# Kernel optimization log

Hardware: AMD Instinct MI355X
Metric: run time of the kernel (lower is better)

The kernel has to match this reference:

```python
import jax, jax.numpy as jnp
import numpy as np

B, N, FEAT = 64, 1024, 3
HID, STATE, LAYERS, NTYPES = 64, 32, 2, 10


def setup_inputs() -> dict:
    key = jax.random.key(0)
    ks = jax.random.split(key, 16)
    s = 0.1
    return {
        "task_features": jax.random.normal(ks[0], (B, N, FEAT), jnp.float32),
        "task_types": jax.random.randint(ks[1], (B, N), 0, NTYPES, jnp.int32),
        "prev_state": jnp.zeros((B, STATE), jnp.float32),
        "enc_w1": jax.random.normal(ks[2], (HID, FEAT), jnp.float32) * s,
        "enc_b1": jnp.zeros((HID,), jnp.float32),
        "enc_w2": jax.random.normal(ks[3], (HID, HID), jnp.float32) * s,
        "enc_b2": jnp.zeros((HID,), jnp.float32),
        "contention": jax.random.normal(ks[4], (NTYPES, NTYPES), jnp.float32) * 0.1,
        "gnn_w": jax.random.normal(ks[5], (LAYERS, HID, HID), jnp.float32) * s,
        "gnn_b": jnp.zeros((LAYERS, HID), jnp.float32),
        "gru_w_ih": jax.random.normal(ks[6], (3 * STATE, HID), jnp.float32) * s,
        "gru_w_hh": jax.random.normal(ks[7], (3 * STATE, STATE), jnp.float32) * s,
        "gru_b_ih": jnp.zeros((3 * STATE,), jnp.float32),
        "gru_b_hh": jnp.zeros((3 * STATE,), jnp.float32),
        "head_w1": jax.random.normal(ks[8], (HID, HID + STATE), jnp.float32) * s,
        "head_b1": jnp.zeros((HID,), jnp.float32),
        "head_w2": jax.random.normal(ks[9], (1, HID), jnp.float32) * s,
        "head_b2": jnp.zeros((1,), jnp.float32),
    }


def _forward(task_features, task_types, prev_state, enc_w1, enc_b1, enc_w2, enc_b2,
             contention, gnn_w, gnn_b, gru_w_ih, gru_w_hh, gru_b_ih, gru_b_hh,
             head_w1, head_b1, head_w2, head_b2):
    # task encoder: Linear -> ReLU -> Linear
    emb = jax.nn.relu(task_features @ enc_w1.T + enc_b1) @ enc_w2.T + enc_b2  # (B,N,H)
    # interaction graph: type-pair gather + cosine similarity
    base = contention[task_types[:, :, None], task_types[:, None, :]]  # (B,N,N)
    nrm = emb / jnp.maximum(jnp.linalg.norm(emb, axis=-1, keepdims=True), 1e-12)
    sim = jnp.einsum("bnd,bmd->bnm", nrm, nrm)
    adjacency = jax.nn.sigmoid(base) * sim  # (B,N,N)
    # GNN layers: aggregate + linear + relu
    h = emb
    for l in range(LAYERS):
        agg = jnp.einsum("bnm,bmd->bnd", adjacency, h)
        h = jax.nn.relu((h + agg) @ gnn_w[l].T + gnn_b[l])
    ctx = h.mean(axis=1)  # (B,H)
    # GRUCell (torch semantics)
    gi = ctx @ gru_w_ih.T + gru_b_ih
    gh = prev_state @ gru_w_hh.T + gru_b_hh
    i_r, i_z, i_n = jnp.split(gi, 3, axis=-1)
    h_r, h_z, h_n = jnp.split(gh, 3, axis=-1)
    r = jax.nn.sigmoid(i_r + h_r)
    z = jax.nn.sigmoid(i_z + h_z)
    n = jnp.tanh(i_n + r * h_n)
    new_state = (1.0 - z) * n + z * prev_state  # (B,S)
    # latency head on [h, state]
    st = jnp.broadcast_to(new_state[:, None, :], (h.shape[0], h.shape[1], new_state.shape[-1]))
    combined = jnp.concatenate([h, st], axis=-1)
    lat = jax.nn.relu(combined @ head_w1.T + head_b1) @ head_w2.T + head_b2
    return lat[..., 0], new_state


def reference(task_features, task_types, prev_state, enc_w1, enc_b1, enc_w2, enc_b2,
              contention, gnn_w, gnn_b, gru_w_ih, gru_w_hh, gru_b_ih, gru_b_hh,
              head_w1, head_b1, head_w2, head_b2):
    return _forward(task_features, task_types, prev_state, enc_w1, enc_b1, enc_w2, enc_b2,
                    contention, gnn_w, gnn_b, gru_w_ih, gru_w_hh, gru_b_ih, gru_b_hh,
                    head_w1, head_b1, head_w2, head_b2)
```

## Files before the change

kernel.cpp:

```cpp
#include <hip/hip_runtime.h>
#include <math.h>

#define BB 64
#define NN 1024
#define HID 64
#define STATE 32
#define NTYPES 10
#define CAP 256
#define CAPE (CAP * 64)

typedef _Float16 f16;
typedef f16 f16x8 __attribute__((ext_vector_type(8)));
typedef f16 f16x4 __attribute__((ext_vector_type(4)));
typedef float f32x4 __attribute__((ext_vector_type(4)));

#define MFMA16(a, b, c) __builtin_amdgcn_mfma_f32_16x16x32_f16(a, b, c, 0, 0, 0)

__device__ __forceinline__ float sigm(float x) { return 1.f / (1.f + expf(-x)); }

__device__ __forceinline__ f16x8 cvt8(float4 a, float4 b) {
    f16x8 r;
    r[0] = (f16)a.x; r[1] = (f16)a.y; r[2] = (f16)a.z; r[3] = (f16)a.w;
    r[4] = (f16)b.x; r[5] = (f16)b.y; r[6] = (f16)b.z; r[7] = (f16)b.w;
    return r;
}
__device__ __forceinline__ unsigned packh2(f16 a, f16 b) {
    union { f16 h[2]; unsigned u; } p;
    p.h[0] = a; p.h[1] = b;
    return p.u;
}

__global__ __launch_bounds__(256) void k_prep(
    const float* __restrict__ w2, const float* __restrict__ gw,
    const float* __restrict__ hw1, f16* __restrict__ out,
    int* __restrict__ cnt, float* __restrict__ ctx)
{
    int p = blockIdx.x * 256 + threadIdx.x;
    if (p < 18432) {
        const float* W; int K, pl;
        if (p < 12288) { int seg = p >> 12; pl = p & 4095; W = (seg == 0) ? w2 : gw + (seg - 1) * 4096; K = 64; }
        else { W = hw1; K = 96; pl = p - 12288; }
        int j = pl & 7, lane = (pl >> 3) & 63, nt = (pl >> 9) & 3, ch = pl >> 11;
        int k = ch * 32 + ((lane >> 4) << 3) + j;
        int o = nt * 16 + (lane & 15);
        out[p] = (f16)W[o * K + k];
        return;
    }
    int q = p - 18432;
    if (q < BB * NTYPES) { cnt[q] = 0; return; }
    q -= BB * NTYPES;
    if (q < BB * HID) ctx[q] = 0.f;
}

__global__ __launch_bounds__(256) void k_encoder(
    const float* __restrict__ feat,
    const float* __restrict__ w1, const float* __restrict__ b1,
    const f16* __restrict__ w2f, const float* __restrict__ b2,
    const int* __restrict__ types, int* __restrict__ idx, int* __restrict__ cnt,
    f16* __restrict__ nrmp, float* __restrict__ sclp)
{
    __shared__ f16 w2s[4096];
    __shared__ f16 tmp[4][16 * 72];
    __shared__ float fbuf[4][48];
    __shared__ int pkbuf[64];
    int tid = threadIdx.x, wave = tid >> 6, lane = tid & 63;
    int l15 = lane & 15, quad = lane >> 4;
    if (tid < 64) {
        int row = blockIdx.x * 64 + tid;
        int b = row >> 10;
        int t = types[row];
        int bt = b * NTYPES + t;
        int pos = atomicAdd(&cnt[bt], 1);
        idx[bt * CAP + pos] = row & (NN - 1);
        pkbuf[tid] = bt * CAP + pos;
    }
    { const uint4* s = (const uint4*)w2f; uint4* d = (uint4*)w2s;
      for (int i = tid; i < 512; i += 256) d[i] = s[i]; }
    float w10 = w1[lane * 3], w11 = w1[lane * 3 + 1], w12 = w1[lane * 3 + 2], b1l = b1[lane];
    int tb = blockIdx.x * 64 + wave * 16;
    if (lane < 48) fbuf[wave][lane] = feat[tb * 3 + lane];
    __syncthreads();
    f16* tw = &tmp[wave][0];
#pragma unroll
    for (int r = 0; r < 16; ++r) {
        float x0 = fbuf[wave][r * 3], x1 = fbuf[wave][r * 3 + 1], x2 = fbuf[wave][r * 3 + 2];
        float hv = fmaxf(fmaf(w10, x0, fmaf(w11, x1, fmaf(w12, x2, b1l))), 0.f);
        tw[r * 72 + lane] = (f16)hv;
    }
    __builtin_amdgcn_sched_barrier(0);
    f16x8 a0 = *(const f16x8*)&tw[l15 * 72 + quad * 8];
    f16x8 a1 = *(const f16x8*)&tw[l15 * 72 + 32 + quad * 8];
    const f16x8* bf = (const f16x8*)w2s;
    f32x4 acc[4];
#pragma unroll
    for (int nt = 0; nt < 4; ++nt) {
        f32x4 c = {0.f, 0.f, 0.f, 0.f};
        c = MFMA16(a0, bf[(0 * 4 + nt) * 64 + lane], c);
        c = MFMA16(a1, bf[(1 * 4 + nt) * 64 + lane], c);
        acc[nt] = c;
    }
    float b2c[4];
#pragma unroll
    for (int nt = 0; nt < 4; ++nt) b2c[nt] = b2[nt * 16 + l15];
#pragma unroll
    for (int i = 0; i < 4; ++i) {
        float v[4]; float ss = 0.f;
#pragma unroll
        for (int nt = 0; nt < 4; ++nt) { v[nt] = acc[nt][i] + b2c[nt]; ss = fmaf(v[nt], v[nt], ss); }
        ss += __shfl_xor(ss, 1, 64); ss += __shfl_xor(ss, 2, 64);
        ss += __shfl_xor(ss, 4, 64); ss += __shfl_xor(ss, 8, 64);
        float nm = fmaxf(sqrtf(ss), 1e-12f);
        float rinv = 1.f / nm;
        int pk = pkbuf[wave * 16 + quad * 4 + i];
#pragma unroll
        for (int nt = 0; nt < 4; ++nt)
            nrmp[(size_t)pk * 64 + nt * 16 + l15] = (f16)(v[nt] * rinv);
        if (l15 == 0) sclp[pk] = nm;
    }
}

#define TSTR2 72
__global__ __launch_bounds__(256) void k_buildM0(
    const int* __restrict__ cnt, const f16* __restrict__ nrmp,
    const float* __restrict__ sclp, f16* __restrict__ M0)
{
    __shared__ f16 nT[64 * TSTR2];
    __shared__ f16 hT[64 * TSTR2];
    int i0 = blockIdx.x;
    int xcd = i0 & 7, kk = i0 >> 3;
    int b = xcd + 8 * (kk / NTYPES);
    int t = kk % NTYPES;
    int bt = b * NTYPES + t;
    int c = cnt[bt];
    int tid = threadIdx.x, wave = tid >> 6, lane = tid & 63;
    int l15 = lane & 15, quad = lane >> 4;
    int r = tid & 15, q4 = tid >> 4;
    const f16* nb = nrmp + (size_t)bt * CAPE;
    const float* sb = sclp + (size_t)bt * CAP;
    f32x4 acc[4] = {{0.f,0.f,0.f,0.f},{0.f,0.f,0.f,0.f},{0.f,0.f,0.f,0.f},{0.f,0.f,0.f,0.f}};
    for (int k0 = 0; k0 < c; k0 += 64) {
        __syncthreads();
        f16x4 a[4], g[4];
#pragma unroll
        for (int u = 0; u < 4; ++u) { a[u] = (f16x4){0,0,0,0}; g[u] = (f16x4){0,0,0,0}; }
#pragma unroll
        for (int u = 0; u < 4; ++u) {
            int mi = k0 + 4 * r + u;
            if (mi < c) {
                a[u] = *(const f16x4*)&nb[(size_t)mi * 64 + 4 * q4];
                f16 sm = (f16)sb[mi]; f16x4 sv = {sm, sm, sm, sm};
                g[u] = a[u] * sv;
            }
        }
#pragma unroll
        for (int i = 0; i < 4; ++i) {
            *(unsigned*)&nT[(4 * q4 + i) * TSTR2 + 4 * r]     = packh2(a[0][i], a[1][i]);
            *(unsigned*)&nT[(4 * q4 + i) * TSTR2 + 4 * r + 2] = packh2(a[2][i], a[3][i]);
            *(unsigned*)&hT[(4 * q4 + i) * TSTR2 + 4 * r]     = packh2(g[0][i], g[1][i]);
            *(unsigned*)&hT[(4 * q4 + i) * TSTR2 + 4 * r + 2] = packh2(g[2][i], g[3][i]);
        }
        __syncthreads();
        f16x8 af0 = *(const f16x8*)&nT[(wave * 16 + l15) * TSTR2 + quad * 8];
        f16x8 af1 = *(const f16x8*)&nT[(wave * 16 + l15) * TSTR2 + 32 + quad * 8];
#pragma unroll
        for (int nt = 0; nt < 4; ++nt) {
            f16x8 bf0 = *(const f16x8*)&hT[(nt * 16 + l15) * TSTR2 + quad * 8];
            f16x8 bf1 = *(const f16x8*)&hT[(nt * 16 + l15) * TSTR2 + 32 + quad * 8];
            acc[nt] = MFMA16(af0, bf0, acc[nt]);
            acc[nt] = MFMA16(af1, bf1, acc[nt]);
        }
    }
    f16* Mo = M0 + (size_t)bt * 4096;
#pragma unroll
    for (int nt = 0; nt < 4; ++nt)
#pragma unroll
        for (int i = 0; i < 4; ++i)
            Mo[(wave * 16 + quad * 4 + i) * 64 + nt * 16 + l15] = (f16)acc[nt][i];
}

__global__ __launch_bounds__(256) void k_gnn0_fused(
    const int* __restrict__ cnt, const float* __restrict__ cont,
    const f16* __restrict__ M, const f16* __restrict__ nrmp,
    const float* __restrict__ sclp,
    const f16* __restrict__ gwf, const float* __restrict__ gb,
    f16* __restrict__ h1p, f16* __restrict__ Mout)
{
    __shared__ f16 ds_[4096];
    __shared__ f16 gs[4096];
    __shared__ __align__(16) f16 nT[64 * TSTR2];
    __shared__ __align__(16) f16 hT[64 * TSTR2];
    int i0 = blockIdx.x;
    int xcd = i0 & 7, kk = i0 >> 3;
    int b = xcd + 8 * (kk / NTYPES);
    int t = kk % NTYPES;
    int bt = b * NTYPES + t;
    int c = cnt[bt];
    int tid = threadIdx.x, wave = tid >> 6, lane = tid & 63;
    int l15 = lane & 15, quad = lane >> 4;
    { const uint4* s2 = (const uint4*)gwf; uint4* d2 = (uint4*)gs;
      for (int i = tid; i < 512; i += 256) d2[i] = s2[i]; }
    float sg[NTYPES];
#pragma unroll
    for (int j = 0; j < NTYPES; ++j) sg[j] = sigm(cont[t * NTYPES + j]);
    float ca[16];
#pragma unroll
    for (int i = 0; i < 16; ++i) ca[i] = 0.f;
    const f16* Mb = M + (size_t)b * NTYPES * 4096;
#pragma unroll
    for (int j = 0; j < NTYPES; ++j) {
        const f16* Mr = Mb + j * 4096 + (wave * 16 + l15) * 64;
        f16x8 m0 = *(const f16x8*)&Mr[quad * 8];
        f16x8 m1 = *(const f16x8*)&Mr[32 + quad * 8];
        float sv = sg[j];
#pragma unroll
        for (int e = 0; e < 8; ++e) {
            ca[e]     = fmaf(sv, (float)m0[e], ca[e]);
            ca[8 + e] = fmaf(sv, (float)m1[e], ca[8 + e]);
        }
    }
    f16x8 ca0, ca1;
#pragma unroll
    for (int i = 0; i < 8; ++i) { ca0[i] = (f16)ca[i]; ca1[i] = (f16)ca[8 + i]; }
    __syncthreads();
    const f16x8* gbf = (const f16x8*)gs;
#pragma unroll
    for (int nt = 0; nt < 4; ++nt) {
        f32x4 dd = {0.f, 0.f, 0.f, 0.f};
        dd = MFMA16(ca0, gbf[(0 * 4 + nt) * 64 + lane], dd);
        dd = MFMA16(ca1, gbf[(1 * 4 + nt) * 64 + lane], dd);
#pragma unroll
        for (int i = 0; i < 4; ++i) {
            int d = wave * 16 + quad * 4 + i;
            int pos = (((d >> 5) * 4 + nt) * 64 + ((d >> 3) & 3) * 16 + l15) * 8 + (d & 7);
            ds_[pos] = (f16)dd[i];
        }
    }
    __syncthreads();
    float gbl[4];
#pragma unroll
    for (int nt = 0; nt < 4; ++nt) gbl[nt] = gb[nt * 16 + l15];
    const f16* nb = nrmp + (size_t)bt * CAPE;
    const float* sb = sclp + (size_t)bt * CAP;
    f16* hob = h1p + (size_t)bt * CAPE;
    const f16x8* dbf = (const f16x8*)ds_;
    f32x4 macc[4];
#pragma unroll
    for (int nt = 0; nt < 4; ++nt) macc[nt] = (f32x4){0.f, 0.f, 0.f, 0.f};
    int nchunk = (c + 63) >> 6;
    for (int ch = 0; ch < nchunk; ++ch) {
        int tb = ch * 64 + wave * 16;
        int rA = tb + l15;
        bool okA = rA < c;
        int rAc = okA ? rA : (c - 1);
        const f16* na = nb + (size_t)rAc * 64;
        f16x8 a0 = *(const f16x8*)&na[quad * 8];
        f16x8 a1 = *(const f16x8*)&na[32 + quad * 8];
        f32x4 acc1[4], acc2[4];
#pragma unroll
        for (int nt = 0; nt < 4; ++nt) {
            f32x4 c1 = {0.f, 0.f, 0.f, 0.f}, c2 = {0.f, 0.f, 0.f, 0.f};
            c1 = MFMA16(a0, dbf[(0 * 4 + nt) * 64 + lane], c1);
            c1 = MFMA16(a1, dbf[(1 * 4 + nt) * 64 + lane], c1);
            c2 = MFMA16(a0, gbf[(0 * 4 + nt) * 64 + lane], c2);
            c2 = MFMA16(a1, gbf[(1 * 4 + nt) * 64 + lane], c2);
            acc1[nt] = c1; acc2[nt] = c2;
        }
        f16x4 hv[4];
#pragma unroll
        for (int nt = 0; nt < 4; ++nt) hv[nt] = (f16x4){0, 0, 0, 0};
#pragma unroll
        for (int i = 0; i < 4; ++i) {
            int rr = tb + quad * 4 + i;
            if (rr < c) {
                float sm = sb[rr];
#pragma unroll
                for (int nt = 0; nt < 4; ++nt) {
                    float v = fmaxf(fmaf(sm, acc2[nt][i], acc1[nt][i]) + gbl[nt], 0.f);
                    f16 vh = (f16)v;
                    hob[(size_t)rr * 64 + nt * 16 + l15] = vh;
                    hv[nt][i] = vh;
                }
            }
        }
        f16x8 z8 = {0, 0, 0, 0, 0, 0, 0, 0};
        f16x8 s0 = okA ? a0 : z8;
        f16x8 s1 = okA ? a1 : z8;
#pragma unroll
        for (int j = 0; j < 8; ++j) {
            nT[(quad * 8 + j) * TSTR2 + wave * 16 + l15]      = s0[j];
            nT[(32 + quad * 8 + j) * TSTR2 + wave * 16 + l15] = s1[j];
        }
#pragma unroll
        for (int nt = 0; nt < 4; ++nt)
            *(f16x4*)&hT[(nt * 16 + l15) * TSTR2 + wave * 16 + quad * 4] = hv[nt];
        __syncthreads();
        f16x8 af0 = *(const f16x8*)&nT[(wave * 16 + l15) * TSTR2 + quad * 8];
        f16x8 af1 = *(const f16x8*)&nT[(wave * 16 + l15) * TSTR2 + 32 + quad * 8];
#pragma unroll
        for (int nt = 0; nt < 4; ++nt) {
            f16x8 bf0 = *(const f16x8*)&hT[(nt * 16 + l15) * TSTR2 + quad * 8];
            f16x8 bf1 = *(const f16x8*)&hT[(nt * 16 + l15) * TSTR2 + 32 + quad * 8];
            macc[nt] = MFMA16(af0, bf0, macc[nt]);
            macc[nt] = MFMA16(af1, bf1, macc[nt]);
        }
        __syncthreads();
    }
    f16* Mo = Mout + (size_t)bt * 4096;
#pragma unroll
    for (int nt = 0; nt < 4; ++nt)
#pragma unroll
        for (int i = 0; i < 4; ++i)
            Mo[(wave * 16 + quad * 4 + i) * 64 + nt * 16 + l15] = (f16)macc[nt][i];
}

__global__ __launch_bounds__(256) void k_gnn1(
    const int* __restrict__ cnt, const float* __restrict__ cont,
    const f16* __restrict__ M, const f16* __restrict__ nrmp,
    const f16* __restrict__ h1p,
    const f16* __restrict__ gwf, const float* __restrict__ gb,
    f16* __restrict__ h2p, float* __restrict__ ctx)
{
    __shared__ f16 ds_[4096];
    __shared__ f16 gs[4096];
    int i0 = blockIdx.x;
    int xcd = i0 & 7, kk = i0 >> 3;
    int b = xcd + 8 * (kk / NTYPES);
    int t = kk % NTYPES;
    int bt = b * NTYPES + t;
    int c = cnt[bt];
    if (c == 0) return;
    int tid = threadIdx.x, wave = tid >> 6, lane = tid & 63;
    int l15 = lane & 15, quad = lane >> 4;
    { const uint4* s2 = (const uint4*)gwf; uint4* d2 = (uint4*)gs;
      for (int i = tid; i < 512; i += 256) d2[i] = s2[i]; }
    float sg[NTYPES];
#pragma unroll
    for (int j = 0; j < NTYPES; ++j) sg[j] = sigm(cont[t * NTYPES + j]);
    float ca[16];
#pragma unroll
    for (int i = 0; i < 16; ++i) ca[i] = 0.f;
    const f16* Mb = M + (size_t)b * NTYPES * 4096;
#pragma unroll
    for (int j = 0; j < NTYPES; ++j) {
        const f16* Mr = Mb + j * 4096 + (wave * 16 + l15) * 64;
        f16x8 m0 = *(const f16x8*)&Mr[quad * 8];
        f16x8 m1 = *(const f16x8*)&Mr[32 + quad * 8];
        float sv = sg[j];
#pragma unroll
        for (int e = 0; e < 8; ++e) {
            ca[e]     = fmaf(sv, (float)m0[e], ca[e]);
            ca[8 + e] = fmaf(sv, (float)m1[e], ca[8 + e]);
        }
    }
    f16x8 ca0, ca1;
#pragma unroll
    for (int i = 0; i < 8; ++i) { ca0[i] = (f16)ca[i]; ca1[i] = (f16)ca[8 + i]; }
    __syncthreads();
    const f16x8* gbf = (const f16x8*)gs;
#pragma unroll
    for (int nt = 0; nt < 4; ++nt) {
        f32x4 dd = {0.f, 0.f, 0.f, 0.f};
        dd = MFMA16(ca0, gbf[(0 * 4 + nt) * 64 + lane], dd);
        dd = MFMA16(ca1, gbf[(1 * 4 + nt) * 64 + lane], dd);
#pragma unroll
        for (int i = 0; i < 4; ++i) {
            int d = wave * 16 + quad * 4 + i;
            int pos = (((d >> 5) * 4 + nt) * 64 + ((d >> 3) & 3) * 16 + l15) * 8 + (d & 7);
            ds_[pos] = (f16)dd[i];
        }
    }
    __syncthreads();
    float gbl[4];
#pragma unroll
    for (int nt = 0; nt < 4; ++nt) gbl[nt] = gb[nt * 16 + l15];
    const f16* nb = nrmp + (size_t)bt * CAPE;
    const f16* hb = h1p + (size_t)bt * CAPE;
    f16* hob = h2p + (size_t)bt * CAPE;
    const f16x8* dbf = (const f16x8*)ds_;
    float cacc[4] = {0.f, 0.f, 0.f, 0.f};
    for (int g = wave; g * 16 < c; g += 4) {
        int tb = g * 16;
        int rA = tb + l15; if (rA >= c) rA = c - 1;
        const f16* na = nb + (size_t)rA * 64;
        f16x8 a0 = *(const f16x8*)&na[quad * 8];
        f16x8 a1 = *(const f16x8*)&na[32 + quad * 8];
        const f16* ha = hb + (size_t)rA * 64;
        f16x8 h0 = *(const f16x8*)&ha[quad * 8];
        f16x8 h1 = *(const f16x8*)&ha[32 + quad * 8];
        f32x4 acc[4];
#pragma unroll
        for (int nt = 0; nt < 4; ++nt) {
            f32x4 cc = {0.f, 0.f, 0.f, 0.f};
            cc = MFMA16(a0, dbf[(0 * 4 + nt) * 64 + lane], cc);
            cc = MFMA16(a1, dbf[(1 * 4 + nt) * 64 + lane], cc);
            cc = MFMA16(h0, gbf[(0 * 4 + nt) * 64 + lane], cc);
            cc = MFMA16(h1, gbf[(1 * 4 + nt) * 64 + lane], cc);
            acc[nt] = cc;
        }
#pragma unroll
        for (int i = 0; i < 4; ++i) {
            int rr = tb + quad * 4 + i;
            if (rr < c) {
#pragma unroll
                for (int nt = 0; nt < 4; ++nt) {
                    float v = fmaxf(acc[nt][i] + gbl[nt], 0.f);
                    hob[(size_t)rr * 64 + nt * 16 + l15] = (f16)v;
                    cacc[nt] += v;
                }
            }
        }
    }
#pragma unroll
    for (int nt = 0; nt < 4; ++nt) {
        float sv = cacc[nt];
        sv += __shfl_xor(sv, 16, 64);
        sv += __shfl_xor(sv, 32, 64);
        if (quad == 0) atomicAdd(&ctx[b * HID + nt * 16 + l15], sv);
    }
}

__global__ __launch_bounds__(256) void k_head(
    const f16* __restrict__ h2p, const int* __restrict__ idx,
    const int* __restrict__ cnt, const float* __restrict__ ctx_sum,
    const float* __restrict__ prev,
    const float* __restrict__ w_ih, const float* __restrict__ w_hh,
    const float* __restrict__ b_ih, const float* __restrict__ b_hh,
    const f16* __restrict__ hwf, const float* __restrict__ b1,
    const float* __restrict__ w2, const float* __restrict__ b2,
    float* __restrict__ lat, float* __restrict__ state_out)
{
    __shared__ f16 ws_[6144];
    __shared__ __align__(16) float st[STATE];
    __shared__ float cs[HID], ps[STATE], gis[96], ghs[96];
    int i0 = blockIdx.x;
    int xcd = i0 & 7, kk = i0 >> 3;
    int b = xcd + 8 * (kk / NTYPES);
    int t = kk % NTYPES;
    int bt = b * NTYPES + t;
    int c = cnt[bt];
    int tid = threadIdx.x, wave = tid >> 6, lane = tid & 63;
    int l15 = lane & 15, quad = lane >> 4;
    { const uint4* s = (const uint4*)hwf; uint4* d = (uint4*)ws_;
      for (int i = tid; i < 768; i += 256) d[i] = s[i]; }
    if (tid < HID) cs[tid] = ctx_sum[b * HID + tid] * (1.f / NN);
    if (tid >= HID && tid < HID + STATE) ps[tid - HID] = prev[b * STATE + tid - HID];
    __syncthreads();
    if (tid < 96) {
        float gi = b_ih[tid];
#pragma unroll 8
        for (int k = 0; k < HID; ++k) gi = fmaf(w_ih[tid * HID + k], cs[k], gi);
        float gh = b_hh[tid];
#pragma unroll
        for (int k = 0; k < STATE; ++k) gh = fmaf(w_hh[tid * STATE + k], ps[k], gh);
        gis[tid] = gi; ghs[tid] = gh;
    }
    __syncthreads();
    if (tid < STATE) {
        float r = sigm(gis[tid] + ghs[tid]);
        float z = sigm(gis[32 + tid] + ghs[32 + tid]);
        float nn = tanhf(gis[64 + tid] + r * ghs[64 + tid]);
        float v = (1.f - z) * nn + z * ps[tid];
        st[tid] = v;
        if (t == 0) state_out[b * STATE + tid] = v;
    }
    __syncthreads();
    if (c == 0) return;
    float b1c[4], w2c[4];
#pragma unroll
    for (int nt = 0; nt < 4; ++nt) { b1c[nt] = b1[nt * 16 + l15]; w2c[nt] = w2[nt * 16 + l15]; }
    float b2v = b2[0];
    const float4* sp = (const float4*)st;
    f16x8 a2 = cvt8(sp[quad * 2], sp[quad * 2 + 1]);
    const f16x8* bf = (const f16x8*)ws_;
    const f16* hb = h2p + (size_t)bt * CAPE;
    const int* lst = idx + (size_t)bt * CAP;
    for (int g = wave; g * 16 < c; g += 4) {
        int tb = g * 16;
        int rA = tb + l15; if (rA >= c) rA = c - 1;
        const f16* ha = hb + (size_t)rA * 64;
        f16x8 a0 = *(const f16x8*)&ha[quad * 8];
        f16x8 a1 = *(const f16x8*)&ha[32 + quad * 8];
        f32x4 acc[4];
#pragma unroll
        for (int nt = 0; nt < 4; ++nt) {
            f32x4 cc = {0.f, 0.f, 0.f, 0.f};
            cc = MFMA16(a0, bf[(0 * 4 + nt) * 64 + lane], cc);
            cc = MFMA16(a1, bf[(1 * 4 + nt) * 64 + lane], cc);
            cc = MFMA16(a2, bf[(2 * 4 + nt) * 64 + lane], cc);
            acc[nt] = cc;
        }
#pragma unroll
        for (int i = 0; i < 4; ++i) {
            float s = 0.f;
#pragma unroll
            for (int nt = 0; nt < 4; ++nt) s = fmaf(fmaxf(acc[nt][i] + b1c[nt], 0.f), w2c[nt], s);
            s += __shfl_xor(s, 1, 64); s += __shfl_xor(s, 2, 64);
            s += __shfl_xor(s, 4, 64); s += __shfl_xor(s, 8, 64);
            int rr = tb + quad * 4 + i;
            if (l15 == 0 && rr < c) {
                int m = lst[rr];
                lat[b * NN + m] = s + b2v;
            }
        }
    }
}

extern "C" void kernel_launch(void* const* d_in, const int* in_sizes, int n_in,
                              void* d_out, int out_size, void* d_ws, size_t ws_size,
                              hipStream_t stream) {
    const float* feat   = (const float*)d_in[0];
    const int*   types  = (const int*)d_in[1];
    const float* prev   = (const float*)d_in[2];
    const float* enc_w1 = (const float*)d_in[3];
    const float* enc_b1 = (const float*)d_in[4];
    const float* enc_w2 = (const float*)d_in[5];
    const float* enc_b2 = (const float*)d_in[6];
    const float* cont   = (const float*)d_in[7];
    const float* gnn_w  = (const float*)d_in[8];
    const float* gnn_b  = (const float*)d_in[9];
    const float* w_ih   = (const float*)d_in[10];
    const float* w_hh   = (const float*)d_in[11];
    const float* b_ih   = (const float*)d_in[12];
    const float* b_hh   = (const float*)d_in[13];
    const float* hw1    = (const float*)d_in[14];
    const float* hb1    = (const float*)d_in[15];
    const float* hw2    = (const float*)d_in[16];
    const float* hb2    = (const float*)d_in[17];
    float* out = (float*)d_out;

    float* ws   = (float*)d_ws;
    f16*   nrmp = (f16*)ws;
    f16*   h1p  = (f16*)(ws + 5242880);
    f16*   h2p  = (f16*)(ws + 10485760);
    float* sclp = ws + 15728640;
    int*   idx  = (int*)(ws + 15892480);
    int*   cnt  = (int*)(ws + 16056320);
    f16*   M0   = (f16*)(ws + 16057344);
    f16*   M1   = (f16*)(ws + 17368064);
    float* ctx  = ws + 18678784;
    f16*   wfrag = (f16*)(ws + 18682880);
    f16*   w2f  = wfrag;
    f16*   gw0f = wfrag + 4096;
    f16*   gw1f = wfrag + 8192;
    f16*   hwf  = wfrag + 12288;

    k_prep<<<91, 256, 0, stream>>>(enc_w2, gnn_w, hw1, wfrag, cnt, ctx);
    k_encoder<<<BB * NN / 64, 256, 0, stream>>>(feat, enc_w1, enc_b1, w2f, enc_b2,
                                                types, idx, cnt, nrmp, sclp);
    k_buildM0<<<BB * NTYPES, 256, 0, stream>>>(cnt, nrmp, sclp, M0);
    k_gnn0_fused<<<BB * NTYPES, 256, 0, stream>>>(cnt, cont, M0, nrmp, sclp,
                                                  gw0f, gnn_b, h1p, M1);
    k_gnn1<<<BB * NTYPES, 256, 0, stream>>>(cnt, cont, M1, nrmp, h1p,
                                            gw1f, gnn_b + HID, h2p, ctx);
    k_head<<<BB * NTYPES, 256, 0, stream>>>(h2p, idx, cnt, ctx, prev,
                                            w_ih, w_hh, b_ih, b_hh,
                                            hwf, hb1, hw2, hb2, out, out + BB * NN);
}
```

Baseline: 165.9 us.

## Recompute per-type M matrices inside GNN kernels and drop buildM0 launch

Removes the separate k_buildM0 kernel and the global M0/M1 buffers. Each (batch,type) block of k_gnn0 and k_gnn1 now recomputes all ten per-type 64x64 Gram matrices for its batch in shared memory, then combines them with the sigmoid contention weights. This saves one launch and the global round trip for M, but every M is now computed ten times, once per type block, so MFMA work and reads of nrmp/h1p grow roughly tenfold.

```diff
diff --git a/kernel.cpp b/kernel.cpp
--- a/kernel.cpp
+++ b/kernel.cpp
@@ -8,6 +8,7 @@
 #define NTYPES 10
 #define CAP 256
 #define CAPE (CAP * 64)
+#define TSTR2 72
 
 typedef _Float16 f16;
 typedef f16 f16x8 __attribute__((ext_vector_type(8)));
@@ -119,71 +120,11 @@
     }
 }
 
-#define TSTR2 72
-__global__ __launch_bounds__(256) void k_buildM0(
-    const int* __restrict__ cnt, const f16* __restrict__ nrmp,
-    const float* __restrict__ sclp, f16* __restrict__ M0)
-{
-    __shared__ f16 nT[64 * TSTR2];
-    __shared__ f16 hT[64 * TSTR2];
-    int i0 = blockIdx.x;
-    int xcd = i0 & 7, kk = i0 >> 3;
-    int b = xcd + 8 * (kk / NTYPES);
-    int t = kk % NTYPES;
-    int bt = b * NTYPES + t;
-    int c = cnt[bt];
-    int tid = threadIdx.x, wave = tid >> 6, lane = tid & 63;
-    int l15 = lane & 15, quad = lane >> 4;
-    int r = tid & 15, q4 = tid >> 4;
-    const f16* nb = nrmp + (size_t)bt * CAPE;
-    const float* sb = sclp + (size_t)bt * CAP;
-    f32x4 acc[4] = {{0.f,0.f,0.f,0.f},{0.f,0.f,0.f,0.f},{0.f,0.f,0.f,0.f},{0.f,0.f,0.f,0.f}};
-    for (int k0 = 0; k0 < c; k0 += 64) {
-        __syncthreads();
-        f16x4 a[4], g[4];
-#pragma unroll
-        for (int u = 0; u < 4; ++u) { a[u] = (f16x4){0,0,0,0}; g[u] = (f16x4){0,0,0,0}; }
-#pragma unroll
-        for (int u = 0; u < 4; ++u) {
-            int mi = k0 + 4 * r + u;
-            if (mi < c) {
-                a[u] = *(const f16x4*)&nb[(size_t)mi * 64 + 4 * q4];
-                f16 sm = (f16)sb[mi]; f16x4 sv = {sm, sm, sm, sm};
-                g[u] = a[u] * sv;
-            }
-        }
-#pragma unroll
-        for (int i = 0; i < 4; ++i) {
-            *(unsigned*)&nT[(4 * q4 + i) * TSTR2 + 4 * r]     = packh2(a[0][i], a[1][i]);
-            *(unsigned*)&nT[(4 * q4 + i) * TSTR2 + 4 * r + 2] = packh2(a[2][i], a[3][i]);
-            *(unsigned*)&hT[(4 * q4 + i) * TSTR2 + 4 * r]     = packh2(g[0][i], g[1][i]);
-            *(unsigned*)&hT[(4 * q4 + i) * TSTR2 + 4 * r + 2] = packh2(g[2][i], g[3][i]);
-        }
-        __syncthreads();
-        f16x8 af0 = *(const f16x8*)&nT[(wave * 16 + l15) * TSTR2 + quad * 8];
-        f16x8 af1 = *(const f16x8*)&nT[(wave * 16 + l15) * TSTR2 + 32 + quad * 8];
-#pragma unroll
-        for (int nt = 0; nt < 4; ++nt) {
-            f16x8 bf0 = *(const f16x8*)&hT[(nt * 16 + l15) * TSTR2 + quad * 8];
-            f16x8 bf1 = *(const f16x8*)&hT[(nt * 16 + l15) * TSTR2 + 32 + quad * 8];
-            acc[nt] = MFMA16(af0, bf0, acc[nt]);
-            acc[nt] = MFMA16(af1, bf1, acc[nt]);
-        }
-    }
-    f16* Mo = M0 + (size_t)bt * 4096;
-#pragma unroll
-    for (int nt = 0; nt < 4; ++nt)
-#pragma unroll
-        for (int i = 0; i < 4; ++i)
-            Mo[(wave * 16 + quad * 4 + i) * 64 + nt * 16 + l15] = (f16)acc[nt][i];
-}
-
-__global__ __launch_bounds__(256) void k_gnn0_fused(
+__global__ __launch_bounds__(256) void k_gnn0(
     const int* __restrict__ cnt, const float* __restrict__ cont,
-    const f16* __restrict__ M, const f16* __restrict__ nrmp,
-    const float* __restrict__ sclp,
+    const f16* __restrict__ nrmp, const float* __restrict__ sclp,
     const f16* __restrict__ gwf, const float* __restrict__ gb,
-    f16* __restrict__ h1p, f16* __restrict__ Mout)
+    f16* __restrict__ h1p)
 {
     __shared__ f16 ds_[4096];
     __shared__ f16 gs[4096];
@@ -195,8 +136,10 @@
     int t = kk % NTYPES;
     int bt = b * NTYPES + t;
     int c = cnt[bt];
+    if (c == 0) return;
     int tid = threadIdx.x, wave = tid >> 6, lane = tid & 63;
     int l15 = lane & 15, quad = lane >> 4;
+    int r = tid & 15, q4 = tid >> 4;
     { const uint4* s2 = (const uint4*)gwf; uint4* d2 = (uint4*)gs;
       for (int i = tid; i < 512; i += 256) d2[i] = s2[i]; }
     float sg[NTYPES];
@@ -205,23 +148,68 @@
     float ca[16];
 #pragma unroll
     for (int i = 0; i < 16; ++i) ca[i] = 0.f;
-    const f16* Mb = M + (size_t)b * NTYPES * 4096;
-#pragma unroll
     for (int j = 0; j < NTYPES; ++j) {
-        const f16* Mr = Mb + j * 4096 + (wave * 16 + l15) * 64;
-        f16x8 m0 = *(const f16x8*)&Mr[quad * 8];
-        f16x8 m1 = *(const f16x8*)&Mr[32 + quad * 8];
-        float sv = sg[j];
-#pragma unroll
-        for (int e = 0; e < 8; ++e) {
-            ca[e]     = fmaf(sv, (float)m0[e], ca[e]);
-            ca[8 + e] = fmaf(sv, (float)m1[e], ca[8 + e]);
-        }
-    }
+        int btj = b * NTYPES + j;
+        int cj = cnt[btj];
+        const f16* nb = nrmp + (size_t)btj * CAPE;
+        const float* sb = sclp + (size_t)btj * CAP;
+        f32x4 macc[4] = {{0.f,0.f,0.f,0.f},{0.f,0.f,0.f,0.f},{0.f,0.f,0.f,0.f},{0.f,0.f,0.f,0.f}};
+        for (int k0 = 0; k0 < cj; k0 += 64) {
+            __syncthreads();
+            f16x4 a[4], g[4];
+#pragma unroll
+            for (int u = 0; u < 4; ++u) { a[u] = (f16x4){0,0,0,0}; g[u] = (f16x4){0,0,0,0}; }
+#pragma unroll
+            for (int u = 0; u < 4; ++u) {
+                int mi = k0 + 4 * r + u;
+                if (mi < cj) {
+                    a[u] = *(const f16x4*)&nb[(size_t)mi * 64 + 4 * q4];
+                    f16 sm = (f16)sb[mi]; f16x4 sv = {sm, sm, sm, sm};
+                    g[u] = a[u] * sv;
+                }
+            }
+#pragma unroll
+            for (int i = 0; i < 4; ++i) {
+                *(unsigned*)&nT[(4 * q4 + i) * TSTR2 + 4 * r]     = packh2(a[0][i], a[1][i]);
+                *(unsigned*)&nT[(4 * q4 + i) * TSTR2 + 4 * r + 2] = packh2(a[2][i], a[3][i]);
+                *(unsigned*)&hT[(4 * q4 + i) * TSTR2 + 4 * r]     = packh2(g[0][i], g[1][i]);
+                *(unsigned*)&hT[(4 * q4 + i) * TSTR2 + 4 * r + 2] = packh2(g[2][i], g[3][i]);
+            }
+            __syncthreads();
+            f16x8 af0 = *(const f16x8*)&nT[(wave * 16 + l15) * TSTR2 + quad * 8];
+            f16x8 af1 = *(const f16x8*)&nT[(wave * 16 + l15) * TSTR2 + 32 + quad * 8];
+#pragma unroll
+            for (int nt = 0; nt < 4; ++nt) {
+                f16x8 bf0 = *(const f16x8*)&hT[(nt * 16 + l15) * TSTR2 + quad * 8];
+                f16x8 bf1 = *(const f16x8*)&hT[(nt * 16 + l15) * TSTR2 + 32 + quad * 8];
+                macc[nt] = MFMA16(af0, bf0, macc[nt]);
+                macc[nt] = MFMA16(af1, bf1, macc[nt]);
+            }
+        }
+        __syncthreads();
+        f16* Mt = nT;
+#pragma unroll
+        for (int nt = 0; nt < 4; ++nt)
+#pragma unroll
+            for (int i = 0; i < 4; ++i)
+                Mt[(wave * 16 + quad * 4 + i) * 64 + nt * 16 + l15] = (f16)macc[nt][i];
+        __syncthreads();
+        {
+            const f16* Mr = Mt + (wave * 16 + l15) * 64;
+            f16x8 m0 = *(const f16x8*)&Mr[quad * 8];
+            f16x8 m1 = *(const f16x8*)&Mr[32 + quad * 8];
+            float sv = sg[j];
+#pragma unroll
+            for (int e = 0; e < 8; ++e) {
+                ca[e]     = fmaf(sv, (float)m0[e], ca[e]);
+                ca[8 + e] = fmaf(sv, (float)m1[e], ca[8 + e]);
+            }
+        }
+    }
+    __syncthreads();
     f16x8 ca0, ca1;
 #pragma unroll
     for (int i = 0; i < 8; ++i) { ca0[i] = (f16)ca[i]; ca1[i] = (f16)ca[8 + i]; }
-    __syncthreads();
     const f16x8* gbf = (const f16x8*)gs;
 #pragma unroll
     for (int nt = 0; nt < 4; ++nt) {
@@ -243,16 +231,10 @@
     const float* sb = sclp + (size_t)bt * CAP;
     f16* hob = h1p + (size_t)bt * CAPE;
     const f16x8* dbf = (const f16x8*)ds_;
-    f32x4 macc[4];
-#pragma unroll
-    for (int nt = 0; nt < 4; ++nt) macc[nt] = (f32x4){0.f, 0.f, 0.f, 0.f};
-    int nchunk = (c + 63) >> 6;
-    for (int ch = 0; ch < nchunk; ++ch) {
-        int tb = ch * 64 + wave * 16;
-        int rA = tb + l15;
-        bool okA = rA < c;
-        int rAc = okA ? rA : (c - 1);
-        const f16* na = nb + (size_t)rAc * 64;
+    for (int g2 = wave; g2 * 16 < c; g2 += 4) {
+        int tb = g2 * 16;
+        int rA = tb + l15; if (rA >= c) rA = c - 1;
+        const f16* na = nb + (size_t)rA * 64;
         f16x8 a0 = *(const f16x8*)&na[quad * 8];
         f16x8 a1 = *(const f16x8*)&na[32 + quad * 8];
         f32x4 acc1[4], acc2[4];
@@ -265,9 +247,6 @@
             c2 = MFMA16(a1, gbf[(1 * 4 + nt) * 64 + lane], c2);
             acc1[nt] = c1; acc2[nt] = c2;
         }
-        f16x4 hv[4];
-#pragma unroll
-        for (int nt = 0; nt < 4; ++nt) hv[nt] = (f16x4){0, 0, 0, 0};
 #pragma unroll
         for (int i = 0; i < 4; ++i) {
             int rr = tb + quad * 4 + i;
@@ -276,52 +255,23 @@
 #pragma unroll
                 for (int nt = 0; nt < 4; ++nt) {
                     float v = fmaxf(fmaf(sm, acc2[nt][i], acc1[nt][i]) + gbl[nt], 0.f);
-                    f16 vh = (f16)v;
-                    hob[(size_t)rr * 64 + nt * 16 + l15] = vh;
-                    hv[nt][i] = vh;
+                    hob[(size_t)rr * 64 + nt * 16 + l15] = (f16)v;
                 }
             }
         }
-        f16x8 z8 = {0, 0, 0, 0, 0, 0, 0, 0};
-        f16x8 s0 = okA ? a0 : z8;
-        f16x8 s1 = okA ? a1 : z8;
-#pragma unroll
-        for (int j = 0; j < 8; ++j) {
-            nT[(quad * 8 + j) * TSTR2 + wave * 16 + l15]      = s0[j];
-            nT[(32 + quad * 8 + j) * TSTR2 + wave * 16 + l15] = s1[j];
-        }
-#pragma unroll
-        for (int nt = 0; nt < 4; ++nt)
-            *(f16x4*)&hT[(nt * 16 + l15) * TSTR2 + wave * 16 + quad * 4] = hv[nt];
-        __syncthreads();
-        f16x8 af0 = *(const f16x8*)&nT[(wave * 16 + l15) * TSTR2 + quad * 8];
-        f16x8 af1 = *(const f16x8*)&nT[(wave * 16 + l15) * TSTR2 + 32 + quad * 8];
-#pragma unroll
-        for (int nt = 0; nt < 4; ++nt) {
-            f16x8 bf0 = *(const f16x8*)&hT[(nt * 16 + l15) * TSTR2 + quad * 8];
-            f16x8 bf1 = *(const f16x8*)&hT[(nt * 16 + l15) * TSTR2 + 32 + quad * 8];
-            macc[nt] = MFMA16(af0, bf0, macc[nt]);
-            macc[nt] = MFMA16(af1, bf1, macc[nt]);
-        }
-        __syncthreads();
-    }
-    f16* Mo = Mout + (size_t)bt * 4096;
-#pragma unroll
-    for (int nt = 0; nt < 4; ++nt)
-#pragma unroll
-        for (int i = 0; i < 4; ++i)
-            Mo[(wave * 16 + quad * 4 + i) * 64 + nt * 16 + l15] = (f16)macc[nt][i];
+    }
 }
 
 __global__ __launch_bounds__(256) void k_gnn1(
     const int* __restrict__ cnt, const float* __restrict__ cont,
-    const f16* __restrict__ M, const f16* __restrict__ nrmp,
-    const f16* __restrict__ h1p,
+    const f16* __restrict__ nrmp, const f16* __restrict__ h1p,
     const f16* __restrict__ gwf, const float* __restrict__ gb,
     f16* __restrict__ h2p, float* __restrict__ ctx)
 {
     __shared__ f16 ds_[4096];
     __shared__ f16 gs[4096];
+    __shared__ __align__(16) f16 nT[64 * TSTR2];
+    __shared__ __align__(16) f16 hT[64 * TSTR2];
     int i0 = blockIdx.x;
     int xcd = i0 & 7, kk = i0 >> 3;
     int b = xcd + 8 * (kk / NTYPES);
@@ -331,6 +281,7 @@
     if (c == 0) return;
     int tid = threadIdx.x, wave = tid >> 6, lane = tid & 63;
     int l15 = lane & 15, quad = lane >> 4;
+    int r = tid & 15, q4 = tid >> 4;
     { const uint4* s2 = (const uint4*)gwf; uint4* d2 = (uint4*)gs;
       for (int i = tid; i < 512; i += 256) d2[i] = s2[i]; }
     float sg[NTYPES];
@@ -339,23 +290,67 @@
     float ca[16];
 #pragma unroll
     for (int i = 0; i < 16; ++i) ca[i] = 0.f;
-    const f16* Mb = M + (size_t)b * NTYPES * 4096;
-#pragma unroll
     for (int j = 0; j < NTYPES; ++j) {
-        const f16* Mr = Mb + j * 4096 + (wave * 16 + l15) * 64;
-        f16x8 m0 = *(const f16x8*)&Mr[quad * 8];
-        f16x8 m1 = *(const f16x8*)&Mr[32 + quad * 8];
-        float sv = sg[j];
-#pragma unroll
-        for (int e = 0; e < 8; ++e) {
-            ca[e]     = fmaf(sv, (float)m0[e], ca[e]);
-            ca[8 + e] = fmaf(sv, (float)m1[e], ca[8 + e]);
-        }
-    }
+        int btj = b * NTYPES + j;
+        int cj = cnt[btj];
+        const f16* nb = nrmp + (size_t)btj * CAPE;
+        const f16* hb = h1p + (size_t)btj * CAPE;
+        f32x4 macc[4] = {{0.f,0.f,0.f,0.f},{0.f,0.f,0.f,0.f},{0.f,0.f,0.f,0.f},{0.f,0.f,0.f,0.f}};
+        for (int k0 = 0; k0 < cj; k0 += 64) {
+            __syncthreads();
+            f16x4 a[4], g[4];
+#pragma unroll
+            for (int u = 0; u < 4; ++u) { a[u] = (f16x4){0,0,0,0}; g[u] = (f16x4){0,0,0,0}; }
+#pragma unroll
+            for (int u = 0; u < 4; ++u) {
+                int mi = k0 + 4 * r + u;
+                if (mi < cj) {
+                    a[u] = *(const f16x4*)&nb[(size_t)mi * 64 + 4 * q4];
+                    g[u] = *(const f16x4*)&hb[(size_t)mi * 64 + 4 * q4];
+                }
+            }
+#pragma unroll
+            for (int i = 0; i < 4; ++i) {
+                *(unsigned*)&nT[(4 * q4 + i) * TSTR2 + 4 * r]     = packh2(a[0][i], a[1][i]);
+                *(unsigned*)&nT[(4 * q4 + i) * TSTR2 + 4 * r + 2] = packh2(a[2][i], a[3][i]);
+                *(unsigned*)&hT[(4 * q4 + i) * TSTR2 + 4 * r]     = packh2(g[0][i], g[1][i]);
+                *(unsigned*)&hT[(4 * q4 + i) * TSTR2 + 4 * r + 2] = packh2(g[2][i], g[3][i]);
+            }
+            __syncthreads();
+            f16x8 af0 = *(const f16x8*)&nT[(wave * 16 + l15) * TSTR2 + quad * 8];
+            f16x8 af1 = *(const f16x8*)&nT[(wave * 16 + l15) * TSTR2 + 32 + quad * 8];
+#pragma unroll
+            for (int nt = 0; nt < 4; ++nt) {
+                f16x8 bf0 = *(const f16x8*)&hT[(nt * 16 + l15) * TSTR2 + quad * 8];
+                f16x8 bf1 = *(const f16x8*)&hT[(nt * 16 + l15) * TSTR2 + 32 + quad * 8];
+                macc[nt] = MFMA16(af0, bf0, macc[nt]);
+                macc[nt] = MFMA16(af1, bf1, macc[nt]);
+            }
+        }
+        __syncthreads();
+        f16* Mt = nT;
+#pragma unroll
+        for (int nt = 0; nt < 4; ++nt)
+#pragma unroll
+            for (int i = 0; i < 4; ++i)
+                Mt[(wave * 16 + quad * 4 + i) * 64 + nt * 16 + l15] = (f16)macc[nt][i];
+        __syncthreads();
+        {
+            const f16* Mr = Mt + (wave * 16 + l15) * 64;
+            f16x8 m0 = *(const f16x8*)&Mr[quad * 8];
+            f16x8 m1 = *(const f16x8*)&Mr[32 + quad * 8];
+            float sv = sg[j];
+#pragma unroll
+            for (int e = 0; e < 8; ++e) {
+                ca[e]     = fmaf(sv, (float)m0[e], ca[e]);
+                ca[8 + e] = fmaf(sv, (float)m1[e], ca[8 + e]);
+            }
+        }
+    }
+    __syncthreads();
     f16x8 ca0, ca1;
 #pragma unroll
     for (int i = 0; i < 8; ++i) { ca0[i] = (f16)ca[i]; ca1[i] = (f16)ca[8 + i]; }
-    __syncthreads();
     const f16x8* gbf = (const f16x8*)gs;
 #pragma unroll
     for (int nt = 0; nt < 4; ++nt) {
@@ -378,8 +373,8 @@
     f16* hob = h2p + (size_t)bt * CAPE;
     const f16x8* dbf = (const f16x8*)ds_;
     float cacc[4] = {0.f, 0.f, 0.f, 0.f};
-    for (int g = wave; g * 16 < c; g += 4) {
-        int tb = g * 16;
+    for (int g2 = wave; g2 * 16 < c; g2 += 4) {
+        int tb = g2 * 16;
         int rA = tb + l15; if (rA >= c) rA = c - 1;
         const f16* na = nb + (size_t)rA * 64;
         f16x8 a0 = *(const f16x8*)&na[quad * 8];
@@ -535,8 +530,6 @@
     float* sclp = ws + 15728640;
     int*   idx  = (int*)(ws + 15892480);
     int*   cnt  = (int*)(ws + 16056320);
-    f16*   M0   = (f16*)(ws + 16057344);
-    f16*   M1   = (f16*)(ws + 17368064);
     float* ctx  = ws + 18678784;
     f16*   wfrag = (f16*)(ws + 18682880);
     f16*   w2f  = wfrag;
@@ -547,10 +540,9 @@
     k_prep<<<91, 256, 0, stream>>>(enc_w2, gnn_w, hw1, wfrag, cnt, ctx);
     k_encoder<<<BB * NN / 64, 256, 0, stream>>>(feat, enc_w1, enc_b1, w2f, enc_b2,
                                                 types, idx, cnt, nrmp, sclp);
-    k_buildM0<<<BB * NTYPES, 256, 0, stream>>>(cnt, nrmp, sclp, M0);
-    k_gnn0_fused<<<BB * NTYPES, 256, 0, stream>>>(cnt, cont, M0, nrmp, sclp,
-                                                  gw0f, gnn_b, h1p, M1);
-    k_gnn1<<<BB * NTYPES, 256, 0, stream>>>(cnt, cont, M1, nrmp, h1p,
+    k_gnn0<<<BB * NTYPES, 256, 0, stream>>>(cnt, cont, nrmp, sclp,
+                                            gw0f, gnn_b, h1p);
+    k_gnn1<<<BB * NTYPES, 256, 0, stream>>>(cnt, cont, nrmp, h1p,
                                             gw1f, gnn_b + HID, h2p, ctx);
     k_head<<<BB * NTYPES, 256, 0, stream>>>(h2p, idx, cnt, ctx, prev,
                                             w_ih, w_hh, b_ih, b_hh,
```

Measured after the change: 226.8 us. 36.7% more time.
